# Optimization experiments

Measured on AMD Instinct MI355X. Metric: run time of the kernel, lower is better.

## Reference

```python
import jax, jax.numpy as jnp
import numpy as np

D_MODEL = 2048
N_EXPERTS = 64
TOP_K = 2
AUX_LOSS_COEF = 0.01
ENTROPY_COEF = 0.01


def setup_inputs() -> dict:
    key = jax.random.key(0)
    kx, kw = jax.random.split(key)
    x = jax.random.normal(kx, (4, 4096, D_MODEL), dtype=jnp.float32)
    # nn.Linear(d_model, n_experts, bias=False) weight: [E, D]
    W = jax.random.normal(kw, (N_EXPERTS, D_MODEL), dtype=jnp.float32) * 0.02
    temp = jnp.ones((1,), dtype=jnp.float32)
    return {"x": x, "W": W, "temp": temp}


def reference(x, W, temp):
    B, S, D = x.shape
    E = W.shape[0]
    # gate logits: [B,S,E]
    logits = jnp.einsum("bsd,ed->bse", x, W)
    t = jnp.clip(temp, 0.1, 5.0)  # self.temp.clamp(0.1, 5.0); eval mode -> no noise
    probs = jax.nn.softmax(logits / t, axis=-1)
    expert_probs, expert_indices = jax.lax.top_k(probs, TOP_K)  # [B,S,K]
    # scatter ones at top-k indices -> [B,S,E]
    expert_mask = jax.nn.one_hot(expert_indices, E, dtype=probs.dtype).sum(axis=-2)
    # aux losses
    importance = probs.mean(axis=(0, 1))                 # [E]
    load = expert_mask.sum(axis=(0, 1)) / (B * S + 1e-6)  # [E]
    aux_load_loss = (importance * load).sum() * E * AUX_LOSS_COEF
    token_entropy = -(probs * jnp.log(jnp.clip(probs, 1e-8))).sum(axis=-1).mean()
    router_entropy = token_entropy * ENTROPY_COEF
    return (expert_probs, expert_indices, expert_mask, aux_load_loss, router_entropy)
```

## Files before the change

kernel.cpp:

```cpp
#include <hip/hip_runtime.h>
#include <hip/hip_bf16.h>
#include <math.h>

#define D_MODEL 2048
#define N_EXP   64
#define NTOK    16384
#define NBLK    512
#define NSTG    16

typedef short bf16x8 __attribute__((ext_vector_type(8)));
typedef float f32x16 __attribute__((ext_vector_type(16)));
typedef unsigned int u32;

#define OFF_PROBS 0
#define OFF_IDX   32768
#define OFF_MASK  65536
#define OFF_AUX   1114112
#define OFF_ENT   1114113

#define WF_PS 16384

#define MEMFENCE asm volatile("" ::: "memory")
#define FULLBAR() do { MEMFENCE; __builtin_amdgcn_s_barrier(); MEMFENCE; \
                       __builtin_amdgcn_sched_barrier(0); } while (0)

__device__ __forceinline__ void split3(float xv, u32& h, u32& m, u32& l) {
  u32 xb = __builtin_bit_cast(u32, xv);
  u32 hb = xb & 0xFFFF0000u;
  float tf = xv - __builtin_bit_cast(float, hb);
  u32 tb = __builtin_bit_cast(u32, tf);
  u32 mb = tb & 0xFFFF0000u;
  float t2 = tf - __builtin_bit_cast(float, mb);
  u32 lb = __builtin_bit_cast(u32, t2);
  h = hb >> 16; m = mb >> 16; l = lb >> 16;
}

__device__ __forceinline__ bool better(float a, int ia, float b, int ib) {
  return (a > b) || (a == b && ia < ib);
}

__global__ __launch_bounds__(256) void wprep_kernel(
    const float* __restrict__ W, bf16x8* __restrict__ Wf) {
  int gid  = blockIdx.x * 256 + threadIdx.x;
  int g    = gid >> 7;
  int n    = (gid >> 6) & 1;
  int lane = gid & 63;
  int e    = n * 32 + (lane & 31);
  int k    = g * 16 + ((lane >> 5) << 3);
  const float* wr = W + (size_t)e * D_MODEL + k;
  bf16x8 hv, mv, lv;
#pragma unroll
  for (int j = 0; j < 8; ++j) {
    u32 h, m, l;
    split3(wr[j], h, m, l);
    hv[j] = (short)h; mv[j] = (short)m; lv[j] = (short)l;
  }
  Wf[gid]             = hv;
  Wf[WF_PS + gid]     = mv;
  Wf[2 * WF_PS + gid] = lv;
}

__global__ __launch_bounds__(512, 4) void fused_kernel(
    const float* __restrict__ x, const bf16x8* __restrict__ Wf,
    const float* __restrict__ temp, float* __restrict__ out,
    float* __restrict__ imp_part, float* __restrict__ load_part,
    float* __restrict__ ent_part) {
  __shared__ float lds[16384];
  const int tid  = threadIdx.x;
  const int w    = tid >> 6;
  const int lane = tid & 63;
  const int t0   = blockIdx.x * 32;
  const int rl   = lane & 31;
  const int hg   = lane >> 5;
  const int st0  = blockIdx.x & 15;

  float tv = temp[0];
  tv = fminf(fmaxf(tv, 0.1f), 5.0f);
  const float invT = 1.0f / tv;

  const float* gsrc[2];
#pragma unroll
  for (int i = 0; i < 2; ++i) {
    int r0  = w * 4 + i * 2;
    int row = r0 + hg;
    int sc  = rl ^ (row & 31);
    gsrc[i] = x + (size_t)(t0 + row) * D_MODEL + sc * 4;
  }

  auto stage = [&](int st) {
    const int buf = st & 3;
    const int kst = (st0 + st) & 15;
#pragma unroll
    for (int i = 0; i < 2; ++i) {
      int r0 = w * 4 + i * 2;
      __builtin_amdgcn_global_load_lds(
          (const __attribute__((address_space(1))) void*)(gsrc[i] + kst * 128),
          (__attribute__((address_space(3))) void*)(lds + buf * 4096 + r0 * 128),
          16, 0, 0);
    }
  };
  auto loadB = [&](int st, bf16x8* bb) {
    const int kst = (st0 + st) & 15;
    const bf16x8* wp = Wf + (size_t)(kst * 8 + w) * 128 + lane;
#pragma unroll
    for (int p = 0; p < 3; ++p)
#pragma unroll
      for (int n = 0; n < 2; ++n)
        bb[p * 2 + n] = wp[p * WF_PS + n * 64];
  };

  f32x16 acc0, acc1;
#pragma unroll
  for (int i = 0; i < 16; ++i) { acc0[i] = 0.0f; acc1[i] = 0.0f; }

  bf16x8 b[2][6];
  stage(0); stage(1);
  loadB(0, b[0]);
  asm volatile("s_waitcnt vmcnt(8)" ::: "memory");
  FULLBAR();

  const int c0 = w * 4 + hg * 2;

#pragma unroll
  for (int st = 0; st < NSTG; ++st) {
    if (st + 1 < NSTG) loadB(st + 1, b[(st + 1) & 1]);
    if (st + 2 < NSTG) stage(st + 2);

    const float* rb = lds + (st & 3) * 4096 + rl * 128;
    float4 a0 = *(const float4*)(rb + ((c0 ^ rl) << 2));
    float4 a1 = *(const float4*)(rb + (((c0 + 1) ^ rl) << 2));
    float av[8] = {a0.x, a0.y, a0.z, a0.w, a1.x, a1.y, a1.z, a1.w};
    bf16x8 ah, am, al;
#pragma unroll
    for (int j = 0; j < 8; ++j) {
      u32 hh, mm, ll;
      split3(av[j], hh, mm, ll);
      ah[j] = (short)hh; am[j] = (short)mm; al[j] = (short)ll;
    }
    const bf16x8* bb = b[st & 1];
    acc0 = __builtin_amdgcn_mfma_f32_32x32x16_bf16(ah, bb[0], acc0, 0, 0, 0);
    acc1 = __builtin_amdgcn_mfma_f32_32x32x16_bf16(ah, bb[1], acc1, 0, 0, 0);
    acc0 = __builtin_amdgcn_mfma_f32_32x32x16_bf16(ah, bb[2], acc0, 0, 0, 0);
    acc1 = __builtin_amdgcn_mfma_f32_32x32x16_bf16(ah, bb[3], acc1, 0, 0, 0);
    acc0 = __builtin_amdgcn_mfma_f32_32x32x16_bf16(am, bb[0], acc0, 0, 0, 0);
    acc1 = __builtin_amdgcn_mfma_f32_32x32x16_bf16(am, bb[1], acc1, 0, 0, 0);
    acc0 = __builtin_amdgcn_mfma_f32_32x32x16_bf16(am, bb[2], acc0, 0, 0, 0);
    acc1 = __builtin_amdgcn_mfma_f32_32x32x16_bf16(am, bb[3], acc1, 0, 0, 0);
    acc0 = __builtin_amdgcn_mfma_f32_32x32x16_bf16(ah, bb[4], acc0, 0, 0, 0);
    acc1 = __builtin_amdgcn_mfma_f32_32x32x16_bf16(ah, bb[5], acc1, 0, 0, 0);
    acc0 = __builtin_amdgcn_mfma_f32_32x32x16_bf16(al, bb[0], acc0, 0, 0, 0);
    acc1 = __builtin_amdgcn_mfma_f32_32x32x16_bf16(al, bb[1], acc1, 0, 0, 0);

    if (st < NSTG - 2) {
      asm volatile("s_waitcnt vmcnt(8)" ::: "memory");
      FULLBAR();
    } else if (st == NSTG - 2) {
      asm volatile("s_waitcnt vmcnt(6)" ::: "memory");
      FULLBAR();
    }
  }

  __syncthreads();
#pragma unroll
  for (int r = 0; r < 16; ++r) {
    int row = (r & 3) + ((r >> 2) << 3) + (hg << 2);
    lds[w * 2048 + row * 64 + rl]      = acc0[r];
    lds[w * 2048 + row * 64 + 32 + rl] = acc1[r];
  }
  __syncthreads();

  const int row  = tid >> 4;
  const int colq = tid & 15;
  float l0 = 0.f, l1 = 0.f, l2 = 0.f, l3 = 0.f;
  for (int wv = 0; wv < 8; ++wv) {
    float4 v = *(const float4*)&lds[wv * 2048 + row * 64 + colq * 4];
    l0 += v.x; l1 += v.y; l2 += v.z; l3 += v.w;
  }
  l0 *= invT; l1 *= invT; l2 *= invT; l3 *= invT;

  float m = fmaxf(fmaxf(l0, l1), fmaxf(l2, l3));
#pragma unroll
  for (int d = 1; d < 16; d <<= 1) m = fmaxf(m, __shfl_xor(m, d));

  float ls0 = l0 - m, ls1 = l1 - m, ls2 = l2 - m, ls3 = l3 - m;
  float e0 = __expf(ls0), e1 = __expf(ls1), e2 = __expf(ls2), e3 = __expf(ls3);
  float ssum = e0 + e1 + e2 + e3;
  float dot  = e0 * ls0 + e1 * ls1 + e2 * ls2 + e3 * ls3;
#pragma unroll
  for (int d = 1; d < 16; d <<= 1) {
    ssum += __shfl_xor(ssum, d);
    dot  += __shfl_xor(dot, d);
  }
  const float inv_s = 1.0f / ssum;
  const float ent = __logf(ssum) - dot * inv_s;

  const int eb = colq * 4;
  float b1 = e0, b2 = -1.0f;
  int   i1 = eb, i2 = eb + 1;
  {
    float ev[3] = {e1, e2, e3};
#pragma unroll
    for (int j = 0; j < 3; ++j) {
      int ej = eb + 1 + j;
      if (better(ev[j], ej, b1, i1)) { b2 = b1; i2 = i1; b1 = ev[j]; i1 = ej; }
      else if (better(ev[j], ej, b2, i2)) { b2 = ev[j]; i2 = ej; }
    }
  }
#pragma unroll
  for (int d = 1; d < 16; d <<= 1) {
    float ob1 = __shfl_xor(b1, d), ob2 = __shfl_xor(b2, d);
    int   oi1 = __shfl_xor(i1, d), oi2 = __shfl_xor(i2, d);
    if (better(ob1, oi1, b1, i1)) {
      if (better(b1, i1, ob2, oi2)) { b2 = b1; i2 = i1; }
      else                          { b2 = ob2; i2 = oi2; }
      b1 = ob1; i1 = oi1;
    } else if (better(ob1, oi1, b2, i2)) {
      b2 = ob1; i2 = oi1;
    }
  }

  const int t = t0 + row;
  if (colq == 0) {
    out[OFF_PROBS + (size_t)t * 2 + 0] = b1 * inv_s;
    out[OFF_PROBS + (size_t)t * 2 + 1] = b2 * inv_s;
    out[OFF_IDX   + (size_t)t * 2 + 0] = (float)i1;
    out[OFF_IDX   + (size_t)t * 2 + 1] = (float)i2;
  }
  {
    float4 mv;
    mv.x = ((eb + 0 == i1) || (eb + 0 == i2)) ? 1.0f : 0.0f;
    mv.y = ((eb + 1 == i1) || (eb + 1 == i2)) ? 1.0f : 0.0f;
    mv.z = ((eb + 2 == i1) || (eb + 2 == i2)) ? 1.0f : 0.0f;
    mv.w = ((eb + 3 == i1) || (eb + 3 == i2)) ? 1.0f : 0.0f;
    *(float4*)&out[OFF_MASK + (size_t)t * N_EXP + eb] = mv;
  }

  __syncthreads();
  {
    float4 p4;
    p4.x = e0 * inv_s; p4.y = e1 * inv_s; p4.z = e2 * inv_s; p4.w = e3 * inv_s;
    *(float4*)&lds[row * 64 + eb] = p4;
  }
  if (colq == 0) {
    lds[2048 + row] = (float)i1;
    lds[2080 + row] = (float)i2;
    lds[2112 + row] = ent;
  }
  __syncthreads();
  if (tid < 64) {
    float simp = 0.0f, sld = 0.0f;
    const float fe = (float)tid;
    for (int r = 0; r < 32; ++r) simp += lds[r * 64 + tid];
    for (int r = 0; r < 32; ++r)
      sld += ((lds[2048 + r] == fe) ? 1.0f : 0.0f)
           + ((lds[2080 + r] == fe) ? 1.0f : 0.0f);
    imp_part[blockIdx.x * N_EXP + tid]  = simp;
    load_part[blockIdx.x * N_EXP + tid] = sld;
    float v = (tid < 32) ? lds[2112 + tid] : 0.0f;
#pragma unroll
    for (int d = 1; d < 64; d <<= 1) v += __shfl_xor(v, d);
    if (tid == 0) ent_part[blockIdx.x] = v;
  }
}

__global__ __launch_bounds__(256) void finalize_part(
    const float* __restrict__ imp_part, const float* __restrict__ load_part,
    const float* __restrict__ ent_part, float* __restrict__ imp2,
    float* __restrict__ load2, float* __restrict__ ent2) {
  __shared__ float si[4][64], sl[4][64], se[4];
  const int tid  = threadIdx.x;
  const int lane = tid & 63;
  const int q    = tid >> 6;
  const int base = blockIdx.x * 8 + q * 2;
  float a = imp_part[(size_t)base * N_EXP + lane]
          + imp_part[(size_t)(base + 1) * N_EXP + lane];
  float b = load_part[(size_t)base * N_EXP + lane]
          + load_part[(size_t)(base + 1) * N_EXP + lane];
  si[q][lane] = a;
  sl[q][lane] = b;
  if (lane == 0) se[q] = ent_part[base] + ent_part[base + 1];
  __syncthreads();
  if (tid < 64) {
    imp2[blockIdx.x * N_EXP + tid]  = si[0][tid] + si[1][tid] + si[2][tid] + si[3][tid];
    load2[blockIdx.x * N_EXP + tid] = sl[0][tid] + sl[1][tid] + sl[2][tid] + sl[3][tid];
    if (tid == 0) ent2[blockIdx.x] = se[0] + se[1] + se[2] + se[3];
  }
}

__global__ __launch_bounds__(256) void finalize_final(
    const float* __restrict__ imp2, const float* __restrict__ load2,
    const float* __restrict__ ent2, float* __restrict__ out) {
  __shared__ float si[4][64], sl[4][64];
  const int tid  = threadIdx.x;
  const int lane = tid & 63;
  const int q    = tid >> 6;
  float a = 0.0f, b = 0.0f;
  for (int r = q * 16; r < q * 16 + 16; ++r) {
    a += imp2[r * N_EXP + lane];
    b += load2[r * N_EXP + lane];
  }
  si[q][lane] = a;
  sl[q][lane] = b;
  __syncthreads();
  if (tid < 64) {
    float imp = si[0][tid] + si[1][tid] + si[2][tid] + si[3][tid];
    float ld  = sl[0][tid] + sl[1][tid] + sl[2][tid] + sl[3][tid];
    imp *= (1.0f / 16384.0f);
    ld  *= (1.0f / (16384.0f + 1e-6f));
    float prod = imp * ld;
    float e = ent2[tid];
#pragma unroll
    for (int d = 1; d < 64; d <<= 1) {
      prod += __shfl_xor(prod, d);
      e    += __shfl_xor(e, d);
    }
    if (tid == 0) {
      out[OFF_AUX] = prod * 64.0f * 0.01f;
      out[OFF_ENT] = (e / 16384.0f) * 0.01f;
    }
  }
}

extern "C" void kernel_launch(void* const* d_in, const int* in_sizes, int n_in,
                              void* d_out, int out_size, void* d_ws, size_t ws_size,
                              hipStream_t stream) {
  const float* x    = (const float*)d_in[0];
  const float* W    = (const float*)d_in[1];
  const float* temp = (const float*)d_in[2];
  float* out = (float*)d_out;
  float* ws  = (float*)d_ws;

  bf16x8* Wf    = (bf16x8*)ws;
  float*  imp   = ws + 196608;
  float*  ldp   = imp + NBLK * N_EXP;
  float*  entp  = ldp + NBLK * N_EXP;
  float*  imp2  = entp + NBLK;
  float*  load2 = imp2 + 64 * N_EXP;
  float*  ent2  = load2 + 64 * N_EXP;

  wprep_kernel<<<64, 256, 0, stream>>>(W, Wf);
  fused_kernel<<<NBLK, 512, 0, stream>>>(x, Wf, temp, out, imp, ldp, entp);
  finalize_part<<<64, 256, 0, stream>>>(imp, ldp, entp, imp2, load2, ent2);
  finalize_final<<<1, 256, 0, stream>>>(imp2, load2, ent2, out);
}
```

Baseline: 44.62 us.

## Process K-stages in pairs with one barrier per pair and deeper prefetch

Restructures the main GEMM loop so two K-stages are handled per iteration. Two A stages are staged into LDS and two B register sets are prefetched, and the LDS barrier plus wait now runs once per pair instead of once per stage. The B loads for a stage are issued right after its MFMAs consume the registers. This halves the number of barriers and keeps more loads in flight, at the cost of more live registers and a deeper reliance on the 4-slot LDS ring. Top-k variables are renamed to avoid clashing with the new b1 buffer.

```diff
diff --git a/kernel.cpp b/kernel.cpp
--- a/kernel.cpp
+++ b/kernel.cpp
@@ -113,20 +113,10 @@
 #pragma unroll
   for (int i = 0; i < 16; ++i) { acc0[i] = 0.0f; acc1[i] = 0.0f; }
 
-  bf16x8 b[2][6];
-  stage(0); stage(1);
-  loadB(0, b[0]);
-  asm volatile("s_waitcnt vmcnt(8)" ::: "memory");
-  FULLBAR();
-
   const int c0 = w * 4 + hg * 2;
 
-#pragma unroll
-  for (int st = 0; st < NSTG; ++st) {
-    if (st + 1 < NSTG) loadB(st + 1, b[(st + 1) & 1]);
-    if (st + 2 < NSTG) stage(st + 2);
-
-    const float* rb = lds + (st & 3) * 4096 + rl * 128;
+  auto dostage = [&](int s, const bf16x8* bb) {
+    const float* rb = lds + (s & 3) * 4096 + rl * 128;
     float4 a0 = *(const float4*)(rb + ((c0 ^ rl) << 2));
     float4 a1 = *(const float4*)(rb + (((c0 + 1) ^ rl) << 2));
     float av[8] = {a0.x, a0.y, a0.z, a0.w, a1.x, a1.y, a1.z, a1.w};
@@ -137,7 +127,6 @@
       split3(av[j], hh, mm, ll);
       ah[j] = (short)hh; am[j] = (short)mm; al[j] = (short)ll;
     }
-    const bf16x8* bb = b[st & 1];
     acc0 = __builtin_amdgcn_mfma_f32_32x32x16_bf16(ah, bb[0], acc0, 0, 0, 0);
     acc1 = __builtin_amdgcn_mfma_f32_32x32x16_bf16(ah, bb[1], acc1, 0, 0, 0);
     acc0 = __builtin_amdgcn_mfma_f32_32x32x16_bf16(ah, bb[2], acc0, 0, 0, 0);
@@ -150,12 +139,28 @@
     acc1 = __builtin_amdgcn_mfma_f32_32x32x16_bf16(ah, bb[5], acc1, 0, 0, 0);
     acc0 = __builtin_amdgcn_mfma_f32_32x32x16_bf16(al, bb[0], acc0, 0, 0, 0);
     acc1 = __builtin_amdgcn_mfma_f32_32x32x16_bf16(al, bb[1], acc1, 0, 0, 0);
-
-    if (st < NSTG - 2) {
-      asm volatile("s_waitcnt vmcnt(8)" ::: "memory");
-      FULLBAR();
-    } else if (st == NSTG - 2) {
-      asm volatile("s_waitcnt vmcnt(6)" ::: "memory");
+  };
+
+  bf16x8 b0[6], b1[6];
+  stage(0); stage(1);
+  loadB(0, b0); loadB(1, b1);
+  asm volatile("s_waitcnt vmcnt(12)" ::: "memory");
+  FULLBAR();
+
+#pragma unroll
+  for (int i = 0; i < 8; ++i) {
+    const int s = 2 * i;
+    const bool more = (s + 2 < NSTG);
+    if (more) { stage(s + 2); stage(s + 3); }
+
+    dostage(s, b0);
+    if (more) loadB(s + 2, b0);
+
+    dostage(s + 1, b1);
+    if (more) loadB(s + 3, b1);
+
+    if (more) {
+      asm volatile("s_waitcnt vmcnt(12)" ::: "memory");
       FULLBAR();
     }
   }
@@ -195,34 +200,34 @@
   const float ent = __logf(ssum) - dot * inv_s;
 
   const int eb = colq * 4;
-  float b1 = e0, b2 = -1.0f;
+  float b1v = e0, b2v = -1.0f;
   int   i1 = eb, i2 = eb + 1;
   {
     float ev[3] = {e1, e2, e3};
 #pragma unroll
     for (int j = 0; j < 3; ++j) {
       int ej = eb + 1 + j;
-      if (better(ev[j], ej, b1, i1)) { b2 = b1; i2 = i1; b1 = ev[j]; i1 = ej; }
-      else if (better(ev[j], ej, b2, i2)) { b2 = ev[j]; i2 = ej; }
+      if (better(ev[j], ej, b1v, i1)) { b2v = b1v; i2 = i1; b1v = ev[j]; i1 = ej; }
+      else if (better(ev[j], ej, b2v, i2)) { b2v = ev[j]; i2 = ej; }
     }
   }
 #pragma unroll
   for (int d = 1; d < 16; d <<= 1) {
-    float ob1 = __shfl_xor(b1, d), ob2 = __shfl_xor(b2, d);
+    float ob1 = __shfl_xor(b1v, d), ob2 = __shfl_xor(b2v, d);
     int   oi1 = __shfl_xor(i1, d), oi2 = __shfl_xor(i2, d);
-    if (better(ob1, oi1, b1, i1)) {
-      if (better(b1, i1, ob2, oi2)) { b2 = b1; i2 = i1; }
-      else                          { b2 = ob2; i2 = oi2; }
-      b1 = ob1; i1 = oi1;
-    } else if (better(ob1, oi1, b2, i2)) {
-      b2 = ob1; i2 = oi1;
+    if (better(ob1, oi1, b1v, i1)) {
+      if (better(b1v, i1, ob2, oi2)) { b2v = b1v; i2 = i1; }
+      else                           { b2v = ob2; i2 = oi2; }
+      b1v = ob1; i1 = oi1;
+    } else if (better(ob1, oi1, b2v, i2)) {
+      b2v = ob1; i2 = oi1;
     }
   }
 
   const int t = t0 + row;
   if (colq == 0) {
-    out[OFF_PROBS + (size_t)t * 2 + 0] = b1 * inv_s;
-    out[OFF_PROBS + (size_t)t * 2 + 1] = b2 * inv_s;
+    out[OFF_PROBS + (size_t)t * 2 + 0] = b1v * inv_s;
+    out[OFF_PROBS + (size_t)t * 2 + 1] = b2v * inv_s;
     out[OFF_IDX   + (size_t)t * 2 + 0] = (float)i1;
     out[OFF_IDX   + (size_t)t * 2 + 1] = (float)i2;
   }
```

New measurement: 47.57 us. 6.6% more time.
